# Performance work log

Hardware: AMD Instinct MI355X
Metric: run time of the kernel (lower is better)

The kernel has to match this reference:

```python
import jax, jax.numpy as jnp
import numpy as np

N, K, D_IN, D_H, D_A, N_CLS = 8192, 10, 1024, 512, 256, 4


def setup_inputs() -> dict:
    key = jax.random.key(0)
    ks = jax.random.split(key, 20)
    def lin(k, fan_in, shape):
        return jax.random.normal(k, shape, dtype=jnp.float32) / np.sqrt(fan_in)
    return {
        "x_path": jax.random.normal(ks[0], (N, D_IN), dtype=jnp.float32),
        "cluster_id": jax.random.randint(ks[1], (N,), 0, K),
        # per-cluster phi MLP (Linear 1024->512, ReLU, Linear 512->512, ReLU); dropout = eval identity
        "W1": lin(ks[2], D_IN, (K, D_IN, D_H)), "b1": jnp.zeros((K, D_H), jnp.float32),
        "W2": lin(ks[3], D_H, (K, D_H, D_H)), "b2": jnp.zeros((K, D_H), jnp.float32),
        # attention_net fc: Linear 512->512 + ReLU
        "fc_W": lin(ks[4], D_H, (D_H, D_H)), "fc_b": jnp.zeros((D_H,), jnp.float32),
        # Attn_Net_Gated: a=tanh(Va), b=sigmoid(Vb), A=(a*b)@Vc
        "Va": lin(ks[5], D_H, (D_H, D_A)), "ba": jnp.zeros((D_A,), jnp.float32),
        "Vb": lin(ks[6], D_H, (D_H, D_A)), "bb": jnp.zeros((D_A,), jnp.float32),
        "Vc": lin(ks[7], D_A, (D_A, 1)), "bc": jnp.zeros((1,), jnp.float32),
        # rho: Linear 512->256 + ReLU
        "rho_W": lin(ks[8], D_H, (D_H, D_A)), "rho_b": jnp.zeros((D_A,), jnp.float32),
        # classifier: Linear 256->4
        "cls_W": lin(ks[9], D_A, (D_A, N_CLS)), "cls_b": jnp.zeros((N_CLS,), jnp.float32),
    }


def reference(x_path, cluster_id, W1, b1, W2, b2, fc_W, fc_b,
              Va, ba, Vb, bb, Vc, bc, rho_W, rho_b, cls_W, cls_b):
    # mask[k, n] = 1 if patch n belongs to cluster k
    mask = (cluster_id[None, :] == jnp.arange(K)[:, None]).astype(x_path.dtype)  # [K, N]

    # per-cluster 2-layer MLP applied to all patches, masked mean-pool (= AdaptiveAvgPool1d(1))
    def phi(W1i, b1i, W2i, b2i):
        h = jax.nn.relu(x_path @ W1i + b1i)          # [N, 512]
        return jax.nn.relu(h @ W2i + b2i)            # [N, 512]
    y = jax.vmap(phi)(W1, b1, W2, b2)                # [K, N, 512]
    cnt = mask.sum(axis=1)                           # [K]
    pooled = jnp.einsum('kn,knd->kd', mask, y) / jnp.maximum(cnt, 1.0)[:, None]  # [K, 512]
    # empty cluster -> zeros (matches torch.zeros((1,512)) branch since b terms are zero via where)
    pooled = jnp.where(cnt[:, None] > 0, pooled, 0.0)

    # attention_net: fc + gated attention
    h = jax.nn.relu(pooled @ fc_W + fc_b)            # [K, 512]
    a = jnp.tanh(h @ Va + ba)                        # [K, 256]
    b = jax.nn.sigmoid(h @ Vb + bb)                  # [K, 256]
    A = (a * b) @ Vc + bc                            # [K, 1]
    A = jax.nn.softmax(A.T, axis=1)                  # [1, K]
    h_path = A @ h                                   # [1, 512]
    h_path = jax.nn.relu(h_path @ rho_W + rho_b)[0]  # [256]
    logits = (h_path @ cls_W + cls_b)[None, :]       # [1, 4]
    Y_hat = jnp.argmax(logits, axis=1, keepdims=True)
    hazards = jax.nn.sigmoid(logits)
    S = jnp.cumprod(1.0 - hazards, axis=1)
    return hazards, S, Y_hat
```

## Files before the change

### kernel.cpp

```cpp
#include <hip/hip_runtime.h>
#include <math.h>

#define NPATCH 8192
#define KC     10
#define DIN    1024
#define DH     512
#define DA     256
#define NCLS   4

#define TM  32
#define LDA 520

typedef unsigned short u16;
typedef short bf16x8 __attribute__((ext_vector_type(8)));
typedef float f32x4  __attribute__((ext_vector_type(4)));

#define OFF_CNT   0
#define OFF_BAR   48
#define OFF_IDX   64
#define OFF_PSUM  327744
#define OFF_H     348224
#define OFF_H2    368768
#define OFF_SRED  369792
#define OFF_W1P   373888
#define OFF_W2P   10859648
#define OFF_H1    16102528

__device__ __forceinline__ u16 f2bf(float f) {
  union { float f; unsigned u; } v; v.f = f;
  unsigned r = (v.u + 0x7fffu + ((v.u >> 16) & 1u)) >> 16;
  return (u16)r;
}

__device__ __forceinline__ unsigned cvtpk(float lo, float hi) {
  unsigned r;
  asm("v_cvt_pk_bf16_f32 %0, %1, %2" : "=v"(r) : "v"(lo), "v"(hi));
  return r;
}

struct __align__(8) U16x4 { u16 x, y, z, w; };
union BF8U { bf16x8 v; unsigned u[4]; };

__device__ __forceinline__ void async16(const void* gp, void* lp) {
  __builtin_amdgcn_global_load_lds(
      (const __attribute__((address_space(1))) void*)gp,
      (__attribute__((address_space(3))) void*)lp, 16, 0, 0);
}

#define W1_TILES (KC * (DIN / 32) * (DH / 32))
#define W2_TILES (KC * (DH / 32) * (DH / 32))
#define NB_BUCKET 32
#define NB_PREP (NB_BUCKET + W1_TILES + W2_TILES)

__global__ __launch_bounds__(256) void prep_kernel(
    const int* __restrict__ cid, int* __restrict__ cnt,
    int* __restrict__ idxlist, const float* __restrict__ W1,
    const float* __restrict__ W2, u16* __restrict__ W1p,
    u16* __restrict__ W2p, float* __restrict__ psum) {
  int b = blockIdx.x, t = threadIdx.x;
  if (b < NB_BUCKET) {
    int g = b * 256 + t;
    if (g < KC * DH) psum[g] = 0.f;
    __shared__ int lcnt[KC], lbase[KC];
    if (t < KC) lcnt[t] = 0;
    __syncthreads();
    int n = b * 256 + t;
    int k = cid[n];
    int myoff = atomicAdd(&lcnt[k], 1);
    __syncthreads();
    if (t < KC) lbase[t] = atomicAdd(&cnt[t], lcnt[t]);
    __syncthreads();
    idxlist[k * NPATCH + lbase[k] + myoff] = n;
  } else {
    __shared__ u16 tile[32][33];
    int bb = b - NB_BUCKET;
    const float* src;
    u16* dst;
    if (bb < W1_TILES) {
      int k = bb / 512, rem = bb % 512;
      int kb = rem / 16, n0 = (rem % 16) * 32;
      src = W1 + (size_t)k * DIN * DH + (size_t)kb * 32 * DH + n0;
      dst = W1p + (((size_t)(k * 32 + kb) * 512 + n0) * 32);
    } else {
      int b2 = bb - W1_TILES;
      int k = b2 / 256, rem = b2 % 256;
      int kb = rem / 16, n0 = (rem % 16) * 32;
      src = W2 + (size_t)k * DH * DH + (size_t)kb * 32 * DH + n0;
      dst = W2p + (((size_t)(k * 16 + kb) * 512 + n0) * 32);
    }
    {
      int ki = t >> 3, n4 = (t & 7) * 4;
      float4 v = *(const float4*)&src[(size_t)ki * DH + n4];
      tile[ki][n4 + 0] = f2bf(v.x);
      tile[ki][n4 + 1] = f2bf(v.y);
      tile[ki][n4 + 2] = f2bf(v.z);
      tile[ki][n4 + 3] = f2bf(v.w);
    }
    __syncthreads();
    {
      int n = t >> 3, ki = (t & 7) * 4;
      U16x4 o = {tile[ki + 0][n], tile[ki + 1][n], tile[ki + 2][n],
                 tile[ki + 3][n]};
      *(U16x4*)&dst[(size_t)n * 32 + ki] = o;
    }
  }
}

__global__ __launch_bounds__(256) void phi1_kernel(
    const float* __restrict__ x, const u16* __restrict__ W1p,
    const float* __restrict__ b1, const int* __restrict__ cnt,
    const int* __restrict__ idxlist, u16* __restrict__ h1) {
  const int k = blockIdx.y;
  if (k >= KC) return;
  const int cntk = cnt[k];
  const int base = blockIdx.z * TM;
  if (base >= cntk) return;
  const int nq = blockIdx.x;

  int cbase = 0;
#pragma unroll
  for (int i = 0; i < KC - 1; ++i) cbase += (i < k) ? cnt[i] : 0;

  const int tid = threadIdx.x;
  const int w = tid >> 6, lane = tid & 63;
  const int quad = lane >> 4, l16 = lane & 15;

  __shared__ __align__(16) u16 A_sh[TM * LDA];
  __shared__ int ridx[TM];
  if (tid < TM) {
    int r = base + tid;
    ridx[tid] = (r < cntk) ? idxlist[k * NPATCH + r] : -1;
  }
  __syncthreads();

  const f32x4 zero4 = {0.f, 0.f, 0.f, 0.f};
  f32x4 acc[2][4];
#pragma unroll
  for (int m = 0; m < 2; ++m)
#pragma unroll
    for (int nt = 0; nt < 4; ++nt) acc[m][nt] = zero4;

  for (int kh = 0; kh < 2; ++kh) {
    if (kh) __syncthreads();
#pragma unroll
    for (int rr = 0; rr < 8; ++rr) {
      int r = w * 8 + rr;
      int src = ridx[r];
      BF8U o;
      if (src >= 0) {
        const float4* xp =
            (const float4*)(x + (size_t)src * DIN + kh * 512 + lane * 8);
        float4 v0 = xp[0], v1 = xp[1];
        o.u[0] = cvtpk(v0.x, v0.y);
        o.u[1] = cvtpk(v0.z, v0.w);
        o.u[2] = cvtpk(v1.x, v1.y);
        o.u[3] = cvtpk(v1.z, v1.w);
      } else {
        o.u[0] = 0; o.u[1] = 0; o.u[2] = 0; o.u[3] = 0;
      }
      *(bf16x8*)&A_sh[r * LDA + lane * 8] = o.v;
    }
    __syncthreads();

    const u16* wb = W1p + ((size_t)(k * 32 + kh * 16) * 512 +
                           (nq * 256 + w * 64 + l16)) * 32 + quad * 8;
    bf16x8 B[2][8];
#pragma unroll
    for (int s = 0; s < 2; ++s)
#pragma unroll
      for (int nt = 0; nt < 4; ++nt)
        B[0][s * 4 + nt] = *(const bf16x8*)(wb + (size_t)s * 16384 + nt * 512);
#pragma unroll
    for (int g = 0; g < 8; ++g) {
      const int cur = g & 1, nxt = cur ^ 1;
      if (g < 7) {
#pragma unroll
        for (int s = 0; s < 2; ++s)
#pragma unroll
          for (int nt = 0; nt < 4; ++nt)
            B[nxt][s * 4 + nt] = *(const bf16x8*)(
                wb + (size_t)((g + 1) * 2 + s) * 16384 + nt * 512);
      }
#pragma unroll
      for (int s = 0; s < 2; ++s) {
        const int ks = g * 2 + s;
        bf16x8 af0 = *(const bf16x8*)&A_sh[l16 * LDA + ks * 32 + quad * 8];
        bf16x8 af1 =
            *(const bf16x8*)&A_sh[(16 + l16) * LDA + ks * 32 + quad * 8];
#pragma unroll
        for (int nt = 0; nt < 4; ++nt) {
          acc[0][nt] = __builtin_amdgcn_mfma_f32_16x16x32_bf16(
              af0, B[cur][s * 4 + nt], acc[0][nt], 0, 0, 0);
          acc[1][nt] = __builtin_amdgcn_mfma_f32_16x16x32_bf16(
              af1, B[cur][s * 4 + nt], acc[1][nt], 0, 0, 0);
        }
      }
    }
  }

  __syncthreads();
#pragma unroll
  for (int m = 0; m < 2; ++m)
#pragma unroll
    for (int nt = 0; nt < 4; ++nt) {
      int c = w * 64 + nt * 16 + l16;
      float bias = b1[k * DH + nq * 256 + c];
#pragma unroll
      for (int r = 0; r < 4; ++r) {
        int row = m * 16 + quad * 4 + r;
        A_sh[row * 264 + c] = f2bf(fmaxf(acc[m][nt][r] + bias, 0.f));
      }
    }
  __syncthreads();
  {
    int row = tid >> 3, seg = tid & 7;
    if (base + row < cntk) {
      u16* dst = h1 + (size_t)(cbase + base + row) * DH + nq * 256 + seg * 32;
#pragma unroll
      for (int j = 0; j < 4; ++j)
        *(bf16x8*)(dst + j * 8) =
            *(const bf16x8*)&A_sh[row * 264 + seg * 32 + j * 8];
    }
  }
}

__global__ __launch_bounds__(256) void phi2_kernel(
    const u16* __restrict__ h1, const u16* __restrict__ W2p,
    const float* __restrict__ b2, const int* __restrict__ cnt,
    float* __restrict__ psum) {
  const int k = blockIdx.y;
  if (k >= KC) return;
  const int cntk = cnt[k];
  const int base = blockIdx.z * TM;
  if (base >= cntk) return;
  const int nq = blockIdx.x;

  int cbase = 0;
#pragma unroll
  for (int i = 0; i < KC - 1; ++i) cbase += (i < k) ? cnt[i] : 0;

  const int tid = threadIdx.x;
  const int w = tid >> 6, lane = tid & 63;
  const int quad = lane >> 4, l16 = lane & 15;

  __shared__ __align__(16) u16 H_sh[TM * LDA];

  const int rowg0 = cbase + base;
  for (int rr = 0; rr < 8; ++rr) {
    int r = w * 8 + rr;
    if (base + r < cntk) {
      async16(h1 + (size_t)(rowg0 + r) * DH + lane * 8, &H_sh[r * LDA]);
    } else {
      bf16x8 z = {0, 0, 0, 0, 0, 0, 0, 0};
      *(bf16x8*)&H_sh[r * LDA + lane * 8] = z;
    }
  }
  __syncthreads();

  const f32x4 zero4 = {0.f, 0.f, 0.f, 0.f};
  f32x4 acc[2][4];
#pragma unroll
  for (int m = 0; m < 2; ++m)
#pragma unroll
    for (int nt = 0; nt < 4; ++nt) acc[m][nt] = zero4;

  const u16* wb = W2p + ((size_t)(k * 16) * 512 +
                         (nq * 256 + w * 64 + l16)) * 32 + quad * 8;
  bf16x8 B[2][8];
#pragma unroll
  for (int s = 0; s < 2; ++s)
#pragma unroll
    for (int nt = 0; nt < 4; ++nt)
      B[0][s * 4 + nt] = *(const bf16x8*)(wb + (size_t)s * 16384 + nt * 512);
#pragma unroll
  for (int g = 0; g < 8; ++g) {
    const int cur = g & 1, nxt = cur ^ 1;
    if (g < 7) {
#pragma unroll
      for (int s = 0; s < 2; ++s)
#pragma unroll
        for (int nt = 0; nt < 4; ++nt)
          B[nxt][s * 4 + nt] = *(const bf16x8*)(
              wb + (size_t)((g + 1) * 2 + s) * 16384 + nt * 512);
    }
#pragma unroll
    for (int s = 0; s < 2; ++s) {
      const int ks = g * 2 + s;
      bf16x8 af0 = *(const bf16x8*)&H_sh[l16 * LDA + ks * 32 + quad * 8];
      bf16x8 af1 =
          *(const bf16x8*)&H_sh[(16 + l16) * LDA + ks * 32 + quad * 8];
#pragma unroll
      for (int nt = 0; nt < 4; ++nt) {
        acc[0][nt] = __builtin_amdgcn_mfma_f32_16x16x32_bf16(
            af0, B[cur][s * 4 + nt], acc[0][nt], 0, 0, 0);
        acc[1][nt] = __builtin_amdgcn_mfma_f32_16x16x32_bf16(
            af1, B[cur][s * 4 + nt], acc[1][nt], 0, 0, 0);
      }
    }
  }

  float vmask[2][4];
#pragma unroll
  for (int m = 0; m < 2; ++m)
#pragma unroll
    for (int r = 0; r < 4; ++r)
      vmask[m][r] = (base + m * 16 + quad * 4 + r < cntk) ? 1.f : 0.f;

#pragma unroll
  for (int nt = 0; nt < 4; ++nt) {
    int col = nq * 256 + w * 64 + nt * 16 + l16;
    float bias = b2[k * DH + col];
    float s = 0.f;
#pragma unroll
    for (int m = 0; m < 2; ++m)
#pragma unroll
      for (int r = 0; r < 4; ++r)
        s += vmask[m][r] * fmaxf(acc[m][nt][r] + bias, 0.f);
    s += __shfl_xor(s, 16, 64);
    s += __shfl_xor(s, 32, 64);
    if (quad == 0) atomicAdd(&psum[k * DH + col], s);
  }
}

#define NTB 64

__device__ __forceinline__ void bar_arrive_wait(int* bar) {
  __syncthreads();
  if (threadIdx.x == 0) {
    __threadfence();
    __hip_atomic_fetch_add(bar, 1, __ATOMIC_RELEASE, __HIP_MEMORY_SCOPE_AGENT);
    while (__hip_atomic_load(bar, __ATOMIC_ACQUIRE,
                             __HIP_MEMORY_SCOPE_AGENT) < NTB) {
      __builtin_amdgcn_s_sleep(1);
    }
  }
  __syncthreads();
}

__global__ __launch_bounds__(256) void tail_kernel(
    const float* __restrict__ psum, const int* __restrict__ cnt,
    const float* __restrict__ fcW, const float* __restrict__ fcb,
    const float* __restrict__ Va, const float* __restrict__ ba,
    const float* __restrict__ Vb, const float* __restrict__ bb_,
    const float* __restrict__ Vc, const float* __restrict__ rhoW,
    const float* __restrict__ rhob, const float* __restrict__ clsW,
    const float* __restrict__ clsb, float* __restrict__ hstore,
    float* __restrict__ sred, float* __restrict__ h2g,
    int* __restrict__ bar, float* __restrict__ out) {
  __shared__ float p_sh[KC * DH];
  __shared__ float r1[2560];
  __shared__ float r2[2560];
  __shared__ float invs[KC];
  __shared__ float gate_sh[4 * KC];
  __shared__ float ws_sh[KC];
  __shared__ float hp_sh[DH];
  const int tid = threadIdx.x;
  const int b = blockIdx.x;

  if (tid < KC) {
    int c = cnt[tid];
    invs[tid] = (c > 0) ? 1.f / (float)c : 0.f;
  }
  __syncthreads();
#pragma unroll
  for (int it = 0; it < KC * DH / 256; ++it) {
    int e = it * 256 + tid;
    p_sh[e] = psum[e] * invs[e >> 9];
  }
  __syncthreads();
  {
    const int jj = tid & 7, dq = tid >> 3;
    const int j0 = b * 8;
    float acc[KC];
#pragma unroll
    for (int k = 0; k < KC; ++k) acc[k] = 0.f;
#pragma unroll 4
    for (int i = 0; i < 16; ++i) {
      int d = dq * 16 + i;
      float wv = fcW[(size_t)d * DH + j0 + jj];
#pragma unroll
      for (int k = 0; k < KC; ++k) acc[k] = fmaf(p_sh[k * DH + d], wv, acc[k]);
    }
#pragma unroll
    for (int k = 0; k < KC; ++k) r1[(dq * 8 + jj) * KC + k] = acc[k];
    __syncthreads();
    if (tid < 8 * KC) {
      int jj2 = tid / KC, k = tid % KC;
      float s = 0.f;
#pragma unroll
      for (int q = 0; q < 32; ++q) s += r1[(q * 8 + jj2) * KC + k];
      hstore[k * DH + j0 + jj2] = fmaxf(s + fcb[j0 + jj2], 0.f);
    }
  }
  bar_arrive_wait(&bar[0]);

#pragma unroll
  for (int it = 0; it < KC * DH / 256; ++it) {
    int e = it * 256 + tid;
    p_sh[e] = hstore[e];
  }
  __syncthreads();
  {
    const int jj = tid & 3, dq = tid >> 2;
    const int j0 = b * 4;
    float sa[KC], sb[KC];
#pragma unroll
    for (int k = 0; k < KC; ++k) { sa[k] = 0.f; sb[k] = 0.f; }
#pragma unroll 4
    for (int i = 0; i < 8; ++i) {
      int d = dq * 8 + i;
      float va = Va[(size_t)d * DA + j0 + jj];
      float vb = Vb[(size_t)d * DA + j0 + jj];
#pragma unroll
      for (int k = 0; k < KC; ++k) {
        float h = p_sh[k * DH + d];
        sa[k] = fmaf(h, va, sa[k]);
        sb[k] = fmaf(h, vb, sb[k]);
      }
    }
#pragma unroll
    for (int k = 0; k < KC; ++k) {
      r1[(dq * 4 + jj) * KC + k] = sa[k];
      r2[(dq * 4 + jj) * KC + k] = sb[k];
    }
    __syncthreads();
    if (tid < 4 * KC) {
      int jj2 = tid / KC, k = tid % KC;
      float ta = 0.f, tb = 0.f;
#pragma unroll
      for (int q = 0; q < 64; ++q) {
        ta += r1[(q * 4 + jj2) * KC + k];
        tb += r2[(q * 4 + jj2) * KC + k];
      }
      float a = tanhf(ta + ba[j0 + jj2]);
      float g = 1.f / (1.f + expf(-(tb + bb_[j0 + jj2])));
      gate_sh[jj2 * KC + k] = a * g * Vc[j0 + jj2];
    }
    __syncthreads();
    if (tid < KC) {
      float s = 0.f;
#pragma unroll
      for (int jj2 = 0; jj2 < 4; ++jj2) s += gate_sh[jj2 * KC + tid];
      sred[b * 16 + tid] = s;
    }
  }
  bar_arrive_wait(&bar[1]);

  if (tid < KC) {
    float s = 0.f;
    for (int q = 0; q < NTB; ++q) s += sred[q * 16 + tid];
    ws_sh[tid] = s;
  }
  __syncthreads();
  if (tid == 0) {
    float m = -1e30f;
#pragma unroll
    for (int k2 = 0; k2 < KC; ++k2) m = fmaxf(m, ws_sh[k2]);
    float Z = 0.f;
#pragma unroll
    for (int k2 = 0; k2 < KC; ++k2) {
      float e = expf(ws_sh[k2] - m);
      ws_sh[k2] = e;
      Z += e;
    }
    float iZ = 1.f / Z;
#pragma unroll
    for (int k2 = 0; k2 < KC; ++k2) ws_sh[k2] *= iZ;
  }
  __syncthreads();
#pragma unroll
  for (int it = 0; it < 2; ++it) {
    int d = it * 256 + tid;
    float s = 0.f;
#pragma unroll
    for (int k2 = 0; k2 < KC; ++k2) s = fmaf(ws_sh[k2], p_sh[k2 * DH + d], s);
    hp_sh[d] = s;
  }
  __syncthreads();
  {
    const int jj = tid & 3, dq = tid >> 2;
    const int j0 = b * 4;
    float acc = 0.f;
#pragma unroll 4
    for (int i = 0; i < 8; ++i) {
      int d = dq * 8 + i;
      acc = fmaf(hp_sh[d], rhoW[(size_t)d * DA + j0 + jj], acc);
    }
    r1[dq * 4 + jj] = acc;
    __syncthreads();
    if (tid < 4) {
      float s = 0.f;
#pragma unroll
      for (int q = 0; q < 64; ++q) s += r1[q * 4 + tid];
      h2g[j0 + tid] = fmaxf(s + rhob[j0 + tid], 0.f);
    }
  }

  if (b != 0) {
    __syncthreads();
    if (tid == 0) {
      __threadfence();
      __hip_atomic_fetch_add(&bar[2], 1, __ATOMIC_RELEASE,
                             __HIP_MEMORY_SCOPE_AGENT);
    }
    return;
  }
  bar_arrive_wait(&bar[2]);
  {
    float h = h2g[tid];
#pragma unroll
    for (int c = 0; c < NCLS; ++c)
      r1[c * 256 + tid] = h * clsW[(size_t)tid * NCLS + c];
    __syncthreads();
    for (int s = 128; s > 0; s >>= 1) {
      if (tid < s) {
#pragma unroll
        for (int c = 0; c < NCLS; ++c)
          r1[c * 256 + tid] += r1[c * 256 + tid + s];
      }
      __syncthreads();
    }
    if (tid == 0) {
      float lg[NCLS], hz[NCLS];
      int best = 0;
#pragma unroll
      for (int c = 0; c < NCLS; ++c) {
        lg[c] = r1[c * 256] + clsb[c];
        hz[c] = 1.f / (1.f + expf(-lg[c]));
        if (lg[c] > lg[best]) best = c;
      }
      float S = 1.f;
#pragma unroll
      for (int c = 0; c < NCLS; ++c) out[c] = hz[c];
#pragma unroll
      for (int c = 0; c < NCLS; ++c) {
        S *= (1.f - hz[c]);
        out[NCLS + c] = S;
      }
      out[2 * NCLS] = (float)best;
    }
  }
}

extern "C" void kernel_launch(void* const* d_in, const int* in_sizes, int n_in,
                              void* d_out, int out_size, void* d_ws,
                              size_t ws_size, hipStream_t stream) {
  const float* x    = (const float*)d_in[0];
  const int*   cid  = (const int*)d_in[1];
  const float* W1   = (const float*)d_in[2];
  const float* b1   = (const float*)d_in[3];
  const float* W2   = (const float*)d_in[4];
  const float* b2   = (const float*)d_in[5];
  const float* fcW  = (const float*)d_in[6];
  const float* fcb  = (const float*)d_in[7];
  const float* Va   = (const float*)d_in[8];
  const float* ba   = (const float*)d_in[9];
  const float* Vb   = (const float*)d_in[10];
  const float* bb_  = (const float*)d_in[11];
  const float* Vc   = (const float*)d_in[12];
  const float* rhoW = (const float*)d_in[14];
  const float* rhob = (const float*)d_in[15];
  const float* clsW = (const float*)d_in[16];
  const float* clsb = (const float*)d_in[17];
  float* out = (float*)d_out;

  char* ws = (char*)d_ws;
  int*   cnt     = (int*)(ws + OFF_CNT);
  int*   bar     = (int*)(ws + OFF_BAR);
  int*   idxlist = (int*)(ws + OFF_IDX);
  float* psum    = (float*)(ws + OFF_PSUM);
  float* hstore  = (float*)(ws + OFF_H);
  float* h2g     = (float*)(ws + OFF_H2);
  float* sred    = (float*)(ws + OFF_SRED);
  u16*   W1p     = (u16*)(ws + OFF_W1P);
  u16*   W2p     = (u16*)(ws + OFF_W2P);
  u16*   h1      = (u16*)(ws + OFF_H1);

  (void)hipMemsetAsync(cnt, 0, 64, stream);
  prep_kernel<<<NB_PREP, 256, 0, stream>>>(cid, cnt, idxlist, W1, W2, W1p, W2p,
                                           psum);
  phi1_kernel<<<dim3(2, 12, NPATCH / TM), 256, 0, stream>>>(x, W1p, b1, cnt,
                                                            idxlist, h1);
  phi2_kernel<<<dim3(2, 12, NPATCH / TM), 256, 0, stream>>>(h1, W2p, b2, cnt,
                                                            psum);
  tail_kernel<<<NTB, 256, 0, stream>>>(psum, cnt, fcW, fcb, Va, ba, Vb, bb_,
                                       Vc, rhoW, rhob, clsW, clsb, hstore,
                                       sred, h2g, bar, out);
}
```

Baseline: 206.3 us.

## Fuse phi1 and phi2 into one persistent kernel keeping h1 in LDS

Merges the two per-cluster MLP layer kernels into a single persistent kernel with 512 blocks of 512 threads. Each block walks a range of 32-row cluster tiles and computes all 512 output columns of layer 1 into LDS, then runs layer 2 from LDS and atomically accumulates the masked pooled sums. This removes the global h1 round trip, one kernel launch and the duplicated x loads across column halves. In exchange each tile is handled by a fixed grid-stride schedule, and LDS use plus register pressure rise, which may limit occupancy.

```diff
diff --git a/kernel.cpp b/kernel.cpp
--- a/kernel.cpp
+++ b/kernel.cpp
@@ -24,7 +24,6 @@
 #define OFF_SRED  369792
 #define OFF_W1P   373888
 #define OFF_W2P   10859648
-#define OFF_H1    16102528
 
 __device__ __forceinline__ u16 f2bf(float f) {
   union { float f; unsigned u; } v; v.f = f;
@@ -40,12 +39,6 @@
 
 struct __align__(8) U16x4 { u16 x, y, z, w; };
 union BF8U { bf16x8 v; unsigned u[4]; };
-
-__device__ __forceinline__ void async16(const void* gp, void* lp) {
-  __builtin_amdgcn_global_load_lds(
-      (const __attribute__((address_space(1))) void*)gp,
-      (__attribute__((address_space(3))) void*)lp, 16, 0, 0);
-}
 
 #define W1_TILES (KC * (DIN / 32) * (DH / 32))
 #define W2_TILES (KC * (DH / 32) * (DH / 32))
@@ -106,45 +99,46 @@
   }
 }
 
-__global__ __launch_bounds__(256) void phi1_kernel(
+__global__ __launch_bounds__(512, 4) void phi_kernel(
     const float* __restrict__ x, const u16* __restrict__ W1p,
-    const float* __restrict__ b1, const int* __restrict__ cnt,
-    const int* __restrict__ idxlist, u16* __restrict__ h1) {
-  const int k = blockIdx.y;
-  if (k >= KC) return;
-  const int cntk = cnt[k];
-  const int base = blockIdx.z * TM;
-  if (base >= cntk) return;
-  const int nq = blockIdx.x;
-
-  int cbase = 0;
-#pragma unroll
-  for (int i = 0; i < KC - 1; ++i) cbase += (i < k) ? cnt[i] : 0;
+    const u16* __restrict__ W2p, const float* __restrict__ b1,
+    const float* __restrict__ b2, const int* __restrict__ cnt,
+    const int* __restrict__ idxlist, float* __restrict__ psum) {
+  __shared__ __align__(16) u16 A0[TM * LDA];
+  __shared__ __align__(16) u16 A1[TM * LDA];
+  __shared__ int ridx[TM];
 
   const int tid = threadIdx.x;
   const int w = tid >> 6, lane = tid & 63;
   const int quad = lane >> 4, l16 = lane & 15;
 
-  __shared__ __align__(16) u16 A_sh[TM * LDA];
-  __shared__ int ridx[TM];
-  if (tid < TM) {
-    int r = base + tid;
-    ridx[tid] = (r < cntk) ? idxlist[k * NPATCH + r] : -1;
-  }
-  __syncthreads();
-
-  const f32x4 zero4 = {0.f, 0.f, 0.f, 0.f};
-  f32x4 acc[2][4];
-#pragma unroll
-  for (int m = 0; m < 2; ++m)
-#pragma unroll
-    for (int nt = 0; nt < 4; ++nt) acc[m][nt] = zero4;
-
-  for (int kh = 0; kh < 2; ++kh) {
-    if (kh) __syncthreads();
-#pragma unroll
-    for (int rr = 0; rr < 8; ++rr) {
-      int r = w * 8 + rr;
+  int cn[KC];
+#pragma unroll
+  for (int i = 0; i < KC; ++i) cn[i] = cnt[i];
+  int G = 0;
+#pragma unroll
+  for (int i = 0; i < KC; ++i) G += (cn[i] + TM - 1) >> 5;
+
+  const int s = blockIdx.x & 7, j = blockIdx.x >> 3;
+  const int lo = (G * s) >> 3, hi = (G * (s + 1)) >> 3;
+
+  for (int g = lo + j; g < hi; g += 64) {
+    int kk = 0, rg = g, cntk = cn[0];
+#pragma unroll
+    for (int i = 0; i < KC - 1; ++i) {
+      int nch = (cn[i] + TM - 1) >> 5;
+      if (rg >= nch) { kk = i + 1; rg -= nch; cntk = cn[i + 1]; }
+    }
+    const int base = rg * TM;
+
+    if (tid < TM)
+      ridx[tid] = (base + tid < cntk) ? idxlist[kk * NPATCH + base + tid] : -1;
+    __syncthreads();
+
+#pragma unroll
+    for (int u8 = 0; u8 < 8; ++u8) {
+      const int kh = u8 & 1;
+      const int r = w * 4 + (u8 >> 1);
       int src = ridx[r];
       BF8U o;
       if (src >= 0) {
@@ -158,167 +152,120 @@
       } else {
         o.u[0] = 0; o.u[1] = 0; o.u[2] = 0; o.u[3] = 0;
       }
-      *(bf16x8*)&A_sh[r * LDA + lane * 8] = o.v;
-    }
-    __syncthreads();
-
-    const u16* wb = W1p + ((size_t)(k * 32 + kh * 16) * 512 +
-                           (nq * 256 + w * 64 + l16)) * 32 + quad * 8;
-    bf16x8 B[2][8];
-#pragma unroll
-    for (int s = 0; s < 2; ++s)
+      u16* dstbuf = kh ? A1 : A0;
+      *(bf16x8*)&dstbuf[r * LDA + lane * 8] = o.v;
+    }
+    __syncthreads();
+
+    const f32x4 zero4 = {0.f, 0.f, 0.f, 0.f};
+    f32x4 acc[2][4];
+#pragma unroll
+    for (int m = 0; m < 2; ++m)
+#pragma unroll
+      for (int nt = 0; nt < 4; ++nt) acc[m][nt] = zero4;
+
+#pragma unroll
+    for (int kh = 0; kh < 2; ++kh) {
+      const u16* Abuf = kh ? A1 : A0;
+      const u16* wb = W1p + ((size_t)(kk * 32 + kh * 16) * 512 +
+                             (w * 64 + l16)) * 32 + quad * 8;
+      bf16x8 B[2][4];
 #pragma unroll
       for (int nt = 0; nt < 4; ++nt)
-        B[0][s * 4 + nt] = *(const bf16x8*)(wb + (size_t)s * 16384 + nt * 512);
-#pragma unroll
-    for (int g = 0; g < 8; ++g) {
-      const int cur = g & 1, nxt = cur ^ 1;
-      if (g < 7) {
-#pragma unroll
-        for (int s = 0; s < 2; ++s)
+        B[0][nt] = *(const bf16x8*)(wb + nt * 512);
+#pragma unroll
+      for (int ks = 0; ks < 16; ++ks) {
+        const int cur = ks & 1, nxt = cur ^ 1;
+        if (ks < 15) {
 #pragma unroll
           for (int nt = 0; nt < 4; ++nt)
-            B[nxt][s * 4 + nt] = *(const bf16x8*)(
-                wb + (size_t)((g + 1) * 2 + s) * 16384 + nt * 512);
-      }
-#pragma unroll
-      for (int s = 0; s < 2; ++s) {
-        const int ks = g * 2 + s;
-        bf16x8 af0 = *(const bf16x8*)&A_sh[l16 * LDA + ks * 32 + quad * 8];
+            B[nxt][nt] =
+                *(const bf16x8*)(wb + (size_t)(ks + 1) * 16384 + nt * 512);
+        }
+        bf16x8 af0 = *(const bf16x8*)&Abuf[l16 * LDA + ks * 32 + quad * 8];
         bf16x8 af1 =
-            *(const bf16x8*)&A_sh[(16 + l16) * LDA + ks * 32 + quad * 8];
+            *(const bf16x8*)&Abuf[(16 + l16) * LDA + ks * 32 + quad * 8];
 #pragma unroll
         for (int nt = 0; nt < 4; ++nt) {
           acc[0][nt] = __builtin_amdgcn_mfma_f32_16x16x32_bf16(
-              af0, B[cur][s * 4 + nt], acc[0][nt], 0, 0, 0);
+              af0, B[cur][nt], acc[0][nt], 0, 0, 0);
           acc[1][nt] = __builtin_amdgcn_mfma_f32_16x16x32_bf16(
-              af1, B[cur][s * 4 + nt], acc[1][nt], 0, 0, 0);
+              af1, B[cur][nt], acc[1][nt], 0, 0, 0);
         }
       }
     }
-  }
-
-  __syncthreads();
-#pragma unroll
-  for (int m = 0; m < 2; ++m)
+    __syncthreads();
+
+#pragma unroll
+    for (int m = 0; m < 2; ++m)
+#pragma unroll
+      for (int nt = 0; nt < 4; ++nt) {
+        int c = w * 64 + nt * 16 + l16;
+        float bias = b1[kk * DH + c];
+#pragma unroll
+        for (int r = 0; r < 4; ++r) {
+          int row = m * 16 + quad * 4 + r;
+          A0[row * LDA + c] = f2bf(fmaxf(acc[m][nt][r] + bias, 0.f));
+        }
+      }
+    __syncthreads();
+
+    f32x4 acc2[2][4];
+#pragma unroll
+    for (int m = 0; m < 2; ++m)
+#pragma unroll
+      for (int nt = 0; nt < 4; ++nt) acc2[m][nt] = zero4;
+
+    {
+      const u16* wb2 = W2p + ((size_t)(kk * 16) * 512 +
+                              (w * 64 + l16)) * 32 + quad * 8;
+      bf16x8 B[2][4];
+#pragma unroll
+      for (int nt = 0; nt < 4; ++nt)
+        B[0][nt] = *(const bf16x8*)(wb2 + nt * 512);
+#pragma unroll
+      for (int ks = 0; ks < 16; ++ks) {
+        const int cur = ks & 1, nxt = cur ^ 1;
+        if (ks < 15) {
+#pragma unroll
+          for (int nt = 0; nt < 4; ++nt)
+            B[nxt][nt] =
+                *(const bf16x8*)(wb2 + (size_t)(ks + 1) * 16384 + nt * 512);
+        }
+        bf16x8 af0 = *(const bf16x8*)&A0[l16 * LDA + ks * 32 + quad * 8];
+        bf16x8 af1 =
+            *(const bf16x8*)&A0[(16 + l16) * LDA + ks * 32 + quad * 8];
+#pragma unroll
+        for (int nt = 0; nt < 4; ++nt) {
+          acc2[0][nt] = __builtin_amdgcn_mfma_f32_16x16x32_bf16(
+              af0, B[cur][nt], acc2[0][nt], 0, 0, 0);
+          acc2[1][nt] = __builtin_amdgcn_mfma_f32_16x16x32_bf16(
+              af1, B[cur][nt], acc2[1][nt], 0, 0, 0);
+        }
+      }
+    }
+
+    float vmask[2][4];
+#pragma unroll
+    for (int m = 0; m < 2; ++m)
+#pragma unroll
+      for (int r = 0; r < 4; ++r)
+        vmask[m][r] = (base + m * 16 + quad * 4 + r < cntk) ? 1.f : 0.f;
+
 #pragma unroll
     for (int nt = 0; nt < 4; ++nt) {
-      int c = w * 64 + nt * 16 + l16;
-      float bias = b1[k * DH + nq * 256 + c];
-#pragma unroll
-      for (int r = 0; r < 4; ++r) {
-        int row = m * 16 + quad * 4 + r;
-        A_sh[row * 264 + c] = f2bf(fmaxf(acc[m][nt][r] + bias, 0.f));
-      }
-    }
-  __syncthreads();
-  {
-    int row = tid >> 3, seg = tid & 7;
-    if (base + row < cntk) {
-      u16* dst = h1 + (size_t)(cbase + base + row) * DH + nq * 256 + seg * 32;
-#pragma unroll
-      for (int j = 0; j < 4; ++j)
-        *(bf16x8*)(dst + j * 8) =
-            *(const bf16x8*)&A_sh[row * 264 + seg * 32 + j * 8];
-    }
-  }
-}
-
-__global__ __launch_bounds__(256) void phi2_kernel(
-    const u16* __restrict__ h1, const u16* __restrict__ W2p,
-    const float* __restrict__ b2, const int* __restrict__ cnt,
-    float* __restrict__ psum) {
-  const int k = blockIdx.y;
-  if (k >= KC) return;
-  const int cntk = cnt[k];
-  const int base = blockIdx.z * TM;
-  if (base >= cntk) return;
-  const int nq = blockIdx.x;
-
-  int cbase = 0;
-#pragma unroll
-  for (int i = 0; i < KC - 1; ++i) cbase += (i < k) ? cnt[i] : 0;
-
-  const int tid = threadIdx.x;
-  const int w = tid >> 6, lane = tid & 63;
-  const int quad = lane >> 4, l16 = lane & 15;
-
-  __shared__ __align__(16) u16 H_sh[TM * LDA];
-
-  const int rowg0 = cbase + base;
-  for (int rr = 0; rr < 8; ++rr) {
-    int r = w * 8 + rr;
-    if (base + r < cntk) {
-      async16(h1 + (size_t)(rowg0 + r) * DH + lane * 8, &H_sh[r * LDA]);
-    } else {
-      bf16x8 z = {0, 0, 0, 0, 0, 0, 0, 0};
-      *(bf16x8*)&H_sh[r * LDA + lane * 8] = z;
-    }
-  }
-  __syncthreads();
-
-  const f32x4 zero4 = {0.f, 0.f, 0.f, 0.f};
-  f32x4 acc[2][4];
-#pragma unroll
-  for (int m = 0; m < 2; ++m)
-#pragma unroll
-    for (int nt = 0; nt < 4; ++nt) acc[m][nt] = zero4;
-
-  const u16* wb = W2p + ((size_t)(k * 16) * 512 +
-                         (nq * 256 + w * 64 + l16)) * 32 + quad * 8;
-  bf16x8 B[2][8];
-#pragma unroll
-  for (int s = 0; s < 2; ++s)
-#pragma unroll
-    for (int nt = 0; nt < 4; ++nt)
-      B[0][s * 4 + nt] = *(const bf16x8*)(wb + (size_t)s * 16384 + nt * 512);
-#pragma unroll
-  for (int g = 0; g < 8; ++g) {
-    const int cur = g & 1, nxt = cur ^ 1;
-    if (g < 7) {
-#pragma unroll
-      for (int s = 0; s < 2; ++s)
-#pragma unroll
-        for (int nt = 0; nt < 4; ++nt)
-          B[nxt][s * 4 + nt] = *(const bf16x8*)(
-              wb + (size_t)((g + 1) * 2 + s) * 16384 + nt * 512);
-    }
-#pragma unroll
-    for (int s = 0; s < 2; ++s) {
-      const int ks = g * 2 + s;
-      bf16x8 af0 = *(const bf16x8*)&H_sh[l16 * LDA + ks * 32 + quad * 8];
-      bf16x8 af1 =
-          *(const bf16x8*)&H_sh[(16 + l16) * LDA + ks * 32 + quad * 8];
-#pragma unroll
-      for (int nt = 0; nt < 4; ++nt) {
-        acc[0][nt] = __builtin_amdgcn_mfma_f32_16x16x32_bf16(
-            af0, B[cur][s * 4 + nt], acc[0][nt], 0, 0, 0);
-        acc[1][nt] = __builtin_amdgcn_mfma_f32_16x16x32_bf16(
-            af1, B[cur][s * 4 + nt], acc[1][nt], 0, 0, 0);
-      }
-    }
-  }
-
-  float vmask[2][4];
-#pragma unroll
-  for (int m = 0; m < 2; ++m)
-#pragma unroll
-    for (int r = 0; r < 4; ++r)
-      vmask[m][r] = (base + m * 16 + quad * 4 + r < cntk) ? 1.f : 0.f;
-
-#pragma unroll
-  for (int nt = 0; nt < 4; ++nt) {
-    int col = nq * 256 + w * 64 + nt * 16 + l16;
-    float bias = b2[k * DH + col];
-    float s = 0.f;
-#pragma unroll
-    for (int m = 0; m < 2; ++m)
-#pragma unroll
-      for (int r = 0; r < 4; ++r)
-        s += vmask[m][r] * fmaxf(acc[m][nt][r] + bias, 0.f);
-    s += __shfl_xor(s, 16, 64);
-    s += __shfl_xor(s, 32, 64);
-    if (quad == 0) atomicAdd(&psum[k * DH + col], s);
+      int col = w * 64 + nt * 16 + l16;
+      float bias = b2[kk * DH + col];
+      float sv = 0.f;
+#pragma unroll
+      for (int m = 0; m < 2; ++m)
+#pragma unroll
+        for (int r = 0; r < 4; ++r)
+          sv += vmask[m][r] * fmaxf(acc2[m][nt][r] + bias, 0.f);
+      sv += __shfl_xor(sv, 16, 64);
+      sv += __shfl_xor(sv, 32, 64);
+      if (quad == 0) atomicAdd(&psum[kk * DH + col], sv);
+    }
   }
 }
 
@@ -515,7 +462,7 @@
     for (int s = 128; s > 0; s >>= 1) {
       if (tid < s) {
 #pragma unroll
-        for (int c = 0; c < NCLS; ++c)
+      for (int c = 0; c < NCLS; ++c)
           r1[c * 256 + tid] += r1[c * 256 + tid + s];
       }
       __syncthreads();
@@ -574,15 +521,11 @@
   float* sred    = (float*)(ws + OFF_SRED);
   u16*   W1p     = (u16*)(ws + OFF_W1P);
   u16*   W2p     = (u16*)(ws + OFF_W2P);
-  u16*   h1      = (u16*)(ws + OFF_H1);
 
   (void)hipMemsetAsync(cnt, 0, 64, stream);
   prep_kernel<<<NB_PREP, 256, 0, stream>>>(cid, cnt, idxlist, W1, W2, W1p, W2p,
                                            psum);
-  phi1_kernel<<<dim3(2, 12, NPATCH / TM), 256, 0, stream>>>(x, W1p, b1, cnt,
-                                                            idxlist, h1);
-  phi2_kernel<<<dim3(2, 12, NPATCH / TM), 256, 0, stream>>>(h1, W2p, b2, cnt,
-                                                            psum);
+  phi_kernel<<<512, 512, 0, stream>>>(x, W1p, W2p, b1, b2, cnt, idxlist, psum);
   tail_kernel<<<NTB, 256, 0, stream>>>(psum, cnt, fcW, fcb, Va, ba, Vb, bb_,
                                        Vc, rhoW, rhob, clsW, clsb, hstore,
                                        sred, h2g, bar, out);
```

Measured after the change: 204.2 us. Within noise of the previous version (-1.0%).
